# Performance work log

Measured on AMD Instinct MI355X. Metric: run time of the kernel, lower is better.

The kernel has to match this reference:

```python
import jax, jax.numpy as jnp
import numpy as np

T, C, H = 2048, 1024, 16
D = C // H  # head dim = 64


def setup_inputs() -> dict:
    key = jax.random.key(0)
    k1, k2, k3 = jax.random.split(key, 3)
    x = jax.random.normal(k1, (T, C), dtype=jnp.float32)
    W_qkv = jax.random.normal(k2, (C, 3 * C), dtype=jnp.float32) * (1.0 / np.sqrt(C))
    b_qkv = jnp.zeros((3 * C,), dtype=jnp.float32)
    W_proj = jax.random.normal(k3, (C, C), dtype=jnp.float32) * (1.0 / np.sqrt(C))
    b_proj = jnp.zeros((C,), dtype=jnp.float32)
    return {"x": x, "W_qkv": W_qkv, "b_qkv": b_qkv, "W_proj": W_proj, "b_proj": b_proj}


def reference(x, W_qkv, b_qkv, W_proj, b_proj):
    t, c = x.shape
    qkv = x @ W_qkv + b_qkv                      # [T, 3C] fused QKV projection
    q, k, v = jnp.split(qkv, 3, axis=-1)         # each [T, C]
    # split heads: [T, C] -> [H, T, D]
    q = q.reshape(t, H, D).transpose(1, 0, 2)
    k = k.reshape(t, H, D).transpose(1, 0, 2)
    v = v.reshape(t, H, D).transpose(1, 0, 2)
    # naive O(T^2) attention, full score matrix [H, T, T]
    att = jnp.einsum('htd,hsd->hts', q, k) / jnp.sqrt(jnp.float32(D))
    att = jax.nn.softmax(att, axis=-1)
    y = jnp.einsum('hts,hsd->htd', att, v)       # [H, T, D]
    y = y.transpose(1, 0, 2).reshape(t, c)       # merge heads -> [T, C]
    return y @ W_proj + b_proj
```

## Files before the change

### kernel.cpp

```cpp
#include <hip/hip_runtime.h>
#include <hip/hip_bf16.h>
#include <stdint.h>

#define T_DIM 2048
#define C_DIM 1024
#define H_DIM 16
#define D_HEAD 64
#define N_QKV 3072
#define CQ 0.18033688011112042f

typedef __bf16 bf16;
typedef __bf16 bf16x8 __attribute__((ext_vector_type(8)));
typedef __bf16 bf16x4 __attribute__((ext_vector_type(4)));
typedef __bf16 bf16x2 __attribute__((ext_vector_type(2)));
typedef float f32x4 __attribute__((ext_vector_type(4)));
typedef short s16x4 __attribute__((ext_vector_type(4)));

__device__ __forceinline__ void lds_load16(const void* g, void* l) {
    __builtin_amdgcn_global_load_lds(
        (const __attribute__((address_space(1))) void*)g,
        (__attribute__((address_space(3))) void*)l, 16, 0, 0);
}

__device__ __forceinline__ f32x4 mfma16(bf16x4 a, bf16x4 b, f32x4 c) {
#if __has_builtin(__builtin_amdgcn_mfma_f32_16x16x16_bf16)
    return __builtin_amdgcn_mfma_f32_16x16x16_bf16(a, b, c, 0, 0, 0);
#elif __has_builtin(__builtin_amdgcn_mfma_f32_16x16x16bf16_1k)
    union { bf16x4 v; s16x4 s; } ua, ub;
    ua.v = a; ub.v = b;
    return __builtin_amdgcn_mfma_f32_16x16x16bf16_1k(ua.s, ub.s, c, 0, 0, 0);
#else
    asm volatile("v_mfma_f32_16x16x16_bf16 %0, %1, %2, %0"
                 : "+v"(c) : "v"(a), "v"(b));
    return c;
#endif
}

__global__ void prep_kernel(const float* __restrict__ x, bf16* __restrict__ xb,
                            const float* __restrict__ Wq, bf16* __restrict__ WqT,
                            const float* __restrict__ Wp, bf16* __restrict__ WpT) {
    __shared__ float tile[32][33];
    int bid = blockIdx.x;
    int t = threadIdx.x;
    if (bid < 1024) {
        int i = (bid * 256 + t) * 8;
        float4 a = *(const float4*)(x + i);
        float4 b = *(const float4*)(x + i + 4);
        bf16x8 o;
        o[0] = (bf16)a.x; o[1] = (bf16)a.y; o[2] = (bf16)a.z; o[3] = (bf16)a.w;
        o[4] = (bf16)b.x; o[5] = (bf16)b.y; o[6] = (bf16)b.z; o[7] = (bf16)b.w;
        *(bf16x8*)(xb + i) = o;
        return;
    }
    bid -= 1024;
    const float* in; bf16* out; int N, nb, kb;
    if (bid < 3072) { in = Wq; out = WqT; N = N_QKV; nb = (bid % 96) * 32; kb = (bid / 96) * 32; }
    else { bid -= 3072; in = Wp; out = WpT; N = C_DIM; nb = (bid % 32) * 32; kb = (bid / 32) * 32; }
    int r = t >> 3, c4 = (t & 7) * 4;
    float4 v = *(const float4*)(in + (size_t)(kb + r) * N + nb + c4);
    tile[r][c4 + 0] = v.x; tile[r][c4 + 1] = v.y;
    tile[r][c4 + 2] = v.z; tile[r][c4 + 3] = v.w;
    __syncthreads();
    bf16x4 ov;
    ov[0] = (bf16)tile[c4 + 0][r]; ov[1] = (bf16)tile[c4 + 1][r];
    ov[2] = (bf16)tile[c4 + 2][r]; ov[3] = (bf16)tile[c4 + 3][r];
    *(bf16x4*)(out + (size_t)(nb + r) * C_DIM + kb + c4) = ov;
}

#define QKV_STAGE(BUF, K0) do {                                                      \
    lds_load16(ga + (K0),                            &As[BUF][0][(w * 16) * 32]);    \
    lds_load16(ga + (K0) + 32,                       &As[BUF][1][(w * 16) * 32]);    \
    lds_load16(ga + (size_t)64 * C_DIM + (K0),       &As[BUF][0][(64 + w * 16) * 32]); \
    lds_load16(ga + (size_t)64 * C_DIM + (K0) + 32,  &As[BUF][1][(64 + w * 16) * 32]); \
    lds_load16(gb + (K0),                            &Bs[BUF][0][(w * 16) * 32]);    \
    lds_load16(gb + (K0) + 32,                       &Bs[BUF][1][(w * 16) * 32]);    \
    lds_load16(gb + (size_t)64 * C_DIM + (K0),       &Bs[BUF][0][(64 + w * 16) * 32]); \
    lds_load16(gb + (size_t)64 * C_DIM + (K0) + 32,  &Bs[BUF][1][(64 + w * 16) * 32]); \
} while (0)

#define QKV_COMPUTE(BUF) do {                                                \
    _Pragma("unroll")                                                        \
    for (int p = 0; p < 2; ++p) {                                            \
        bf16x8 af[4], bfr[4];                                                \
        _Pragma("unroll")                                                    \
        for (int mi = 0; mi < 4; ++mi) af[mi]  = *(const bf16x8*)&As[BUF][p][(wm + mi * 16 + lo16) * 32 + quad * 8]; \
        _Pragma("unroll")                                                    \
        for (int ni = 0; ni < 4; ++ni) bfr[ni] = *(const bf16x8*)&Bs[BUF][p][(wn + ni * 16 + lo16) * 32 + quad * 8]; \
        _Pragma("unroll")                                                    \
        for (int mi = 0; mi < 4; ++mi)                                       \
            _Pragma("unroll")                                                \
            for (int ni = 0; ni < 4; ++ni)                                   \
                acc[mi][ni] = __builtin_amdgcn_mfma_f32_16x16x32_bf16(af[mi], bfr[ni], acc[mi][ni], 0, 0, 0); \
    }                                                                        \
} while (0)

#define WAIT_AND_BARRIER() do {                                              \
    asm volatile("s_waitcnt vmcnt(0)" ::: "memory");                         \
    __builtin_amdgcn_s_barrier();                                            \
} while (0)

__global__ __launch_bounds__(256, 2) void qkv_gemm_kernel(
    const bf16* __restrict__ A, const bf16* __restrict__ Bt,
    const float* __restrict__ bias, bf16* __restrict__ qkv)
{
    __shared__ __align__(16) bf16 As[2][2][128 * 32];
    __shared__ __align__(16) bf16 Bs[2][2][128 * 32];
    const int bid = blockIdx.x;
    const int xcd = bid & 7, slot = bid >> 3;
    const int rowBase = (slot / 3) * 128;
    const int colBase = (xcd * 3 + (slot % 3)) * 128;
    const int tid = threadIdx.x, lane = tid & 63, w = tid >> 6;
    const int lo16 = lane & 15, quad = lane >> 4;
    const int wm = (w & 1) * 64, wn = (w >> 1) * 64;

    const bf16* ga = A  + (size_t)(rowBase + w * 16 + (lane >> 2)) * C_DIM + (lane & 3) * 8;
    const bf16* gb = Bt + (size_t)(colBase + w * 16 + (lane >> 2)) * C_DIM + (lane & 3) * 8;

    f32x4 acc[4][4] = {};

    QKV_STAGE(0, 0);
    WAIT_AND_BARRIER();

    for (int k0 = 0; k0 < C_DIM; k0 += 128) {
        QKV_STAGE(1, k0 + 64);
        QKV_COMPUTE(0);
        WAIT_AND_BARRIER();
        if (k0 + 128 < C_DIM) QKV_STAGE(0, k0 + 128);
        QKV_COMPUTE(1);
        WAIT_AND_BARRIER();
    }

    const float scale = (colBase < C_DIM) ? CQ : 1.0f;
    #pragma unroll
    for (int ni = 0; ni < 4; ++ni) {
        int col = colBase + wn + ni * 16 + lo16;
        float bv = bias[col];
        #pragma unroll
        for (int mi = 0; mi < 4; ++mi) {
            int row0 = rowBase + wm + mi * 16 + quad * 4;
            #pragma unroll
            for (int r = 0; r < 4; ++r)
                qkv[(size_t)(row0 + r) * N_QKV + col] = (bf16)((acc[mi][ni][r] + bv) * scale);
        }
    }
}

#define NKT (T_DIM / 128)

#define FLASH_IT(KT, VC, VN)                                                          \
    {                                                                                 \
        bf16x8 nkf0 = kf0, nkf1 = kf1;                                                \
        if ((KT) + 1 < NKT) {                                                         \
            const bf16* kp = kfb + (size_t)((KT) + 1) * 128 * N_QKV;                  \
            nkf0 = *(const bf16x8*)(kp);                                              \
            nkf1 = *(const bf16x8*)(kp + 32);                                         \
            const bf16* vp = vfb + (size_t)((KT) + 1) * 128 * N_QKV;                  \
            _Pragma("unroll")                                                         \
            for (int mi = 0; mi < 4; ++mi)                                            \
                _Pragma("unroll")                                                     \
                for (int i = 0; i < 4; ++i)                                           \
                    VN[mi][i] = vp[(size_t)i * N_QKV + mi * 16];                      \
        }                                                                             \
        f32x4 st[4];                                                                  \
        __builtin_amdgcn_s_setprio(1);                                                \
        _Pragma("unroll")                                                             \
        for (int nq = 0; nq < 4; ++nq) {                                              \
            f32x4 z = {};                                                             \
            z = __builtin_amdgcn_mfma_f32_16x16x32_bf16(kf0, qf[nq][0], z, 0, 0, 0);  \
            st[nq] = __builtin_amdgcn_mfma_f32_16x16x32_bf16(kf1, qf[nq][1], z, 0, 0, 0); \
        }                                                                             \
        __builtin_amdgcn_s_setprio(0);                                                \
        bf16x4 pb[4];                                                                 \
        _Pragma("unroll")                                                             \
        for (int nq = 0; nq < 4; ++nq)                                                \
            _Pragma("unroll")                                                         \
            for (int r = 0; r < 4; ++r)                                               \
                pb[nq][r] = (bf16)__builtin_amdgcn_exp2f(st[nq][r]);                  \
        __builtin_amdgcn_s_setprio(1);                                                \
        _Pragma("unroll")                                                             \
        for (int nq = 0; nq < 4; ++nq)                                                \
            o_l[nq] = mfma16(pb[nq], ones1, o_l[nq]);                                 \
        _Pragma("unroll")                                                             \
        for (int nq = 0; nq < 4; ++nq)                                                \
            _Pragma("unroll")                                                         \
            for (int mi = 0; mi < 4; ++mi)                                            \
                o_t[nq][mi] = mfma16(pb[nq], VC[mi], o_t[nq][mi]);                    \
        __builtin_amdgcn_s_setprio(0);                                                \
        kf0 = nkf0; kf1 = nkf1;                                                       \
    }

__global__ __launch_bounds__(512, 2) void flash_kernel(
    const bf16* __restrict__ qkv,
    bf16* __restrict__ y)
{
    __shared__ float Ored[8][16][67];
    __shared__ float lred[8][64];

    const int bid = blockIdx.x;
    const int xcd = bid & 7, slot = bid >> 3;
    const int h = xcd * 2 + (slot & 1);
    const int qb = slot >> 1;
    const int tid  = threadIdx.x;
    const int lane = tid & 63, w = tid >> 6;
    const int lo16 = lane & 15, quad = lane >> 4;

    bf16x8 qf[4][2];
    #pragma unroll
    for (int nq = 0; nq < 4; ++nq)
        #pragma unroll
        for (int dk = 0; dk < 2; ++dk)
            qf[nq][dk] = *(const bf16x8*)(qkv + (size_t)(qb * 64 + nq * 16 + lo16) * N_QKV
                                          + h * D_HEAD + dk * 32 + quad * 8);

    f32x4 o_t[4][4] = {};
    f32x4 o_l[4] = {};
    bf16x4 ones1;
    ones1[0] = (bf16)1.0f; ones1[1] = (bf16)1.0f; ones1[2] = (bf16)1.0f; ones1[3] = (bf16)1.0f;

    const bf16* kfb = qkv + (size_t)(w * 16 + lo16) * N_QKV + C_DIM + h * D_HEAD + quad * 8;
    const bf16* vfb = qkv + (size_t)(w * 16 + quad * 4) * N_QKV + 2 * C_DIM + h * D_HEAD + lo16;

    bf16x8 kf0 = *(const bf16x8*)(kfb);
    bf16x8 kf1 = *(const bf16x8*)(kfb + 32);
    bf16x4 vA[4], vB[4];
    #pragma unroll
    for (int mi = 0; mi < 4; ++mi)
        #pragma unroll
        for (int i = 0; i < 4; ++i)
            vA[mi][i] = vfb[(size_t)i * N_QKV + mi * 16];

    for (int kt = 0; kt < NKT; kt += 2) {
        FLASH_IT(kt,     vA, vB);
        FLASH_IT(kt + 1, vB, vA);
    }

    if (lo16 == 0) {
        #pragma unroll
        for (int nq = 0; nq < 4; ++nq)
            #pragma unroll
            for (int i = 0; i < 4; ++i)
                lred[w][nq * 16 + quad * 4 + i] = o_l[nq][i];
    }

    const int qloc = tid >> 5;
    const int d0   = (tid & 31) * 2;
    for (int nq = 0; nq < 4; ++nq) {
        __syncthreads();
        #pragma unroll
        for (int mi = 0; mi < 4; ++mi)
            #pragma unroll
            for (int i = 0; i < 4; ++i)
                Ored[w][quad * 4 + i][mi * 16 + lo16] = o_t[nq][mi][i];
        __syncthreads();
        float ls = 0.f;
        #pragma unroll
        for (int j = 0; j < 8; ++j) ls += lred[j][nq * 16 + qloc];
        float linv = 1.0f / ls;
        float s0 = 0.f, s1 = 0.f;
        #pragma unroll
        for (int j = 0; j < 8; ++j) { s0 += Ored[j][qloc][d0]; s1 += Ored[j][qloc][d0 + 1]; }
        bf16x2 ov;
        ov[0] = (bf16)(s0 * linv); ov[1] = (bf16)(s1 * linv);
        *(bf16x2*)&y[(size_t)(qb * 64 + nq * 16 + qloc) * C_DIM + h * D_HEAD + d0] = ov;
    }
}

#define PROJ_STAGE(BUF, K0) do {                                             \
    lds_load16(ga + (K0),      &As[BUF][0][(w * 16) * 32]);                  \
    lds_load16(ga + (K0) + 32, &As[BUF][1][(w * 16) * 32]);                  \
    lds_load16(gb + (K0),      &Bs[BUF][0][(w * 16) * 32]);                  \
    lds_load16(gb + (K0) + 32, &Bs[BUF][1][(w * 16) * 32]);                  \
} while (0)

#define PROJ_COMPUTE(BUF) do {                                               \
    _Pragma("unroll")                                                        \
    for (int p = 0; p < 2; ++p) {                                            \
        bf16x8 af[2], bfr[2];                                                \
        _Pragma("unroll")                                                    \
        for (int mi = 0; mi < 2; ++mi) af[mi]  = *(const bf16x8*)&As[BUF][p][(wm + mi * 16 + lo16) * 32 + quad * 8]; \
        _Pragma("unroll")                                                    \
        for (int ni = 0; ni < 2; ++ni) bfr[ni] = *(const bf16x8*)&Bs[BUF][p][(wn + ni * 16 + lo16) * 32 + quad * 8]; \
        _Pragma("unroll")                                                    \
        for (int mi = 0; mi < 2; ++mi)                                       \
            _Pragma("unroll")                                                \
            for (int ni = 0; ni < 2; ++ni)                                   \
                acc[mi][ni] = __builtin_amdgcn_mfma_f32_16x16x32_bf16(af[mi], bfr[ni], acc[mi][ni], 0, 0, 0); \
    }                                                                        \
} while (0)

__global__ __launch_bounds__(256, 4) void proj_gemm_kernel(
    const bf16* __restrict__ A, const bf16* __restrict__ Bt,
    const float* __restrict__ bias, float* __restrict__ out)
{
    __shared__ __align__(16) bf16 As[2][2][64 * 32];
    __shared__ __align__(16) bf16 Bs[2][2][64 * 32];
    const int bid = blockIdx.x;
    const int xcd = bid & 7, slot = bid >> 3;
    const int colBase = (xcd * 2 + (slot & 1)) * 64;
    const int rowBase = (slot >> 1) * 64;
    const int tid = threadIdx.x, lane = tid & 63, w = tid >> 6;
    const int lo16 = lane & 15, quad = lane >> 4;
    const int wm = (w & 1) * 32, wn = (w >> 1) * 32;

    const bf16* ga = A  + (size_t)(rowBase + w * 16 + (lane >> 2)) * C_DIM + (lane & 3) * 8;
    const bf16* gb = Bt + (size_t)(colBase + w * 16 + (lane >> 2)) * C_DIM + (lane & 3) * 8;

    f32x4 acc[2][2] = {};

    PROJ_STAGE(0, 0);
    WAIT_AND_BARRIER();

    for (int k0 = 0; k0 < C_DIM; k0 += 128) {
        PROJ_STAGE(1, k0 + 64);
        PROJ_COMPUTE(0);
        WAIT_AND_BARRIER();
        if (k0 + 128 < C_DIM) PROJ_STAGE(0, k0 + 128);
        PROJ_COMPUTE(1);
        WAIT_AND_BARRIER();
    }

    #pragma unroll
    for (int ni = 0; ni < 2; ++ni) {
        int col = colBase + wn + ni * 16 + lo16;
        float bv = bias[col];
        #pragma unroll
        for (int mi = 0; mi < 2; ++mi) {
            int row0 = rowBase + wm + mi * 16 + quad * 4;
            #pragma unroll
            for (int r = 0; r < 4; ++r)
                out[(size_t)(row0 + r) * C_DIM + col] = acc[mi][ni][r] + bv;
        }
    }
}

extern "C" void kernel_launch(void* const* d_in, const int* in_sizes, int n_in,
                              void* d_out, int out_size, void* d_ws, size_t ws_size,
                              hipStream_t stream) {
    const float* x      = (const float*)d_in[0];
    const float* W_qkv  = (const float*)d_in[1];
    const float* b_qkv  = (const float*)d_in[2];
    const float* W_proj = (const float*)d_in[3];
    const float* b_proj = (const float*)d_in[4];
    float* out = (float*)d_out;

    char* ws = (char*)d_ws;
    bf16* xb      = (bf16*)(ws);
    bf16* Wqkv_t  = (bf16*)(ws + (4  << 20));
    bf16* Wproj_t = (bf16*)(ws + (10 << 20));
    bf16* qkv_bf  = (bf16*)(ws + (12 << 20));
    bf16* yb      = (bf16*)(ws + (24 << 20));

    prep_kernel<<<5120, 256, 0, stream>>>(x, xb, W_qkv, Wqkv_t, W_proj, Wproj_t);

    qkv_gemm_kernel<<<384, 256, 0, stream>>>(xb, Wqkv_t, b_qkv, qkv_bf);

    flash_kernel<<<512, 512, 0, stream>>>(qkv_bf, yb);

    proj_gemm_kernel<<<512, 256, 0, stream>>>(yb, Wproj_t, b_proj, out);
}
```

Measured before the change: 150.2 us.

## Write V transposed from QKV GEMM epilogue for vectorized flash V loads

```diff
diff --git a/kernel.cpp b/kernel.cpp
--- a/kernel.cpp
+++ b/kernel.cpp
@@ -101,7 +101,8 @@
 
 __global__ __launch_bounds__(256, 2) void qkv_gemm_kernel(
     const bf16* __restrict__ A, const bf16* __restrict__ Bt,
-    const float* __restrict__ bias, bf16* __restrict__ qkv)
+    const float* __restrict__ bias, bf16* __restrict__ qkv,
+    bf16* __restrict__ vT)
 {
     __shared__ __align__(16) bf16 As[2][2][128 * 32];
     __shared__ __align__(16) bf16 Bs[2][2][128 * 32];
@@ -130,17 +131,34 @@
         WAIT_AND_BARRIER();
     }
 
-    const float scale = (colBase < C_DIM) ? CQ : 1.0f;
-    #pragma unroll
-    for (int ni = 0; ni < 4; ++ni) {
-        int col = colBase + wn + ni * 16 + lo16;
-        float bv = bias[col];
-        #pragma unroll
-        for (int mi = 0; mi < 4; ++mi) {
-            int row0 = rowBase + wm + mi * 16 + quad * 4;
-            #pragma unroll
-            for (int r = 0; r < 4; ++r)
-                qkv[(size_t)(row0 + r) * N_QKV + col] = (bf16)((acc[mi][ni][r] + bv) * scale);
+    if (colBase < 2 * C_DIM) {
+        const float scale = (colBase < C_DIM) ? CQ : 1.0f;
+        #pragma unroll
+        for (int ni = 0; ni < 4; ++ni) {
+            int col = colBase + wn + ni * 16 + lo16;
+            float bv = bias[col];
+            #pragma unroll
+            for (int mi = 0; mi < 4; ++mi) {
+                int row0 = rowBase + wm + mi * 16 + quad * 4;
+                #pragma unroll
+                for (int r = 0; r < 4; ++r)
+                    qkv[(size_t)(row0 + r) * N_QKV + col] = (bf16)((acc[mi][ni][r] + bv) * scale);
+            }
+        }
+    } else {
+        #pragma unroll
+        for (int ni = 0; ni < 4; ++ni) {
+            int col = colBase + wn + ni * 16 + lo16;
+            int vc = col - 2 * C_DIM;
+            float bv = bias[col];
+            #pragma unroll
+            for (int mi = 0; mi < 4; ++mi) {
+                int row0 = rowBase + wm + mi * 16 + quad * 4;
+                bf16x4 ov;
+                #pragma unroll
+                for (int r = 0; r < 4; ++r) ov[r] = (bf16)(acc[mi][ni][r] + bv);
+                *(bf16x4*)&vT[(size_t)vc * T_DIM + row0] = ov;
+            }
         }
     }
 }
@@ -154,12 +172,10 @@
             const bf16* kp = kfb + (size_t)((KT) + 1) * 128 * N_QKV;                  \
             nkf0 = *(const bf16x8*)(kp);                                              \
             nkf1 = *(const bf16x8*)(kp + 32);                                         \
-            const bf16* vp = vfb + (size_t)((KT) + 1) * 128 * N_QKV;                  \
+            const bf16* vp = vfb + ((KT) + 1) * 128;                                  \
             _Pragma("unroll")                                                         \
             for (int mi = 0; mi < 4; ++mi)                                            \
-                _Pragma("unroll")                                                     \
-                for (int i = 0; i < 4; ++i)                                           \
-                    VN[mi][i] = vp[(size_t)i * N_QKV + mi * 16];                      \
+                VN[mi] = *(const bf16x4*)(vp + mi * 16 * T_DIM);                      \
         }                                                                             \
         f32x4 st[4];                                                                  \
         __builtin_amdgcn_s_setprio(1);                                                \
@@ -191,6 +207,7 @@
 
 __global__ __launch_bounds__(512, 2) void flash_kernel(
     const bf16* __restrict__ qkv,
+    const bf16* __restrict__ vT,
     bf16* __restrict__ y)
 {
     __shared__ float Ored[8][16][67];
@@ -218,16 +235,14 @@
     ones1[0] = (bf16)1.0f; ones1[1] = (bf16)1.0f; ones1[2] = (bf16)1.0f; ones1[3] = (bf16)1.0f;
 
     const bf16* kfb = qkv + (size_t)(w * 16 + lo16) * N_QKV + C_DIM + h * D_HEAD + quad * 8;
-    const bf16* vfb = qkv + (size_t)(w * 16 + quad * 4) * N_QKV + 2 * C_DIM + h * D_HEAD + lo16;
+    const bf16* vfb = vT + ((size_t)h * D_HEAD + lo16) * T_DIM + w * 16 + quad * 4;
 
     bf16x8 kf0 = *(const bf16x8*)(kfb);
     bf16x8 kf1 = *(const bf16x8*)(kfb + 32);
     bf16x4 vA[4], vB[4];
     #pragma unroll
     for (int mi = 0; mi < 4; ++mi)
-        #pragma unroll
-        for (int i = 0; i < 4; ++i)
-            vA[mi][i] = vfb[(size_t)i * N_QKV + mi * 16];
+        vA[mi] = *(const bf16x4*)(vfb + mi * 16 * T_DIM);
 
     for (int kt = 0; kt < NKT; kt += 2) {
         FLASH_IT(kt,     vA, vB);
@@ -349,12 +364,13 @@
     bf16* Wproj_t = (bf16*)(ws + (10 << 20));
     bf16* qkv_bf  = (bf16*)(ws + (12 << 20));
     bf16* yb      = (bf16*)(ws + (24 << 20));
+    bf16* vT      = (bf16*)(ws + (28 << 20));
 
     prep_kernel<<<5120, 256, 0, stream>>>(x, xb, W_qkv, Wqkv_t, W_proj, Wproj_t);
 
-    qkv_gemm_kernel<<<384, 256, 0, stream>>>(xb, Wqkv_t, b_qkv, qkv_bf);
-
-    flash_kernel<<<512, 512, 0, stream>>>(qkv_bf, yb);
+    qkv_gemm_kernel<<<384, 256, 0, stream>>>(xb, Wqkv_t, b_qkv, qkv_bf, vT);
+
+    flash_kernel<<<512, 512, 0, stream>>>(qkv_bf, vT, yb);
 
     proj_gemm_kernel<<<512, 256, 0, stream>>>(yb, Wproj_t, b_proj, out);
 }
```

Result: slower. 169.6 us (+12.9%).

## Rebalance QKV GEMM tiles, fold W_proj transpose into it, shrink flash blocks

Applied to the files above, without the earlier changes.

```diff
diff --git a/kernel.cpp b/kernel.cpp
--- a/kernel.cpp
+++ b/kernel.cpp
@@ -37,8 +37,7 @@
 }
 
 __global__ void prep_kernel(const float* __restrict__ x, bf16* __restrict__ xb,
-                            const float* __restrict__ Wq, bf16* __restrict__ WqT,
-                            const float* __restrict__ Wp, bf16* __restrict__ WpT) {
+                            const float* __restrict__ Wq, bf16* __restrict__ WqT) {
     __shared__ float tile[32][33];
     int bid = blockIdx.x;
     int t = threadIdx.x;
@@ -53,18 +52,16 @@
         return;
     }
     bid -= 1024;
-    const float* in; bf16* out; int N, nb, kb;
-    if (bid < 3072) { in = Wq; out = WqT; N = N_QKV; nb = (bid % 96) * 32; kb = (bid / 96) * 32; }
-    else { bid -= 3072; in = Wp; out = WpT; N = C_DIM; nb = (bid % 32) * 32; kb = (bid / 32) * 32; }
+    int nb = (bid % 96) * 32, kb = (bid / 96) * 32;
     int r = t >> 3, c4 = (t & 7) * 4;
-    float4 v = *(const float4*)(in + (size_t)(kb + r) * N + nb + c4);
+    float4 v = *(const float4*)(Wq + (size_t)(kb + r) * N_QKV + nb + c4);
     tile[r][c4 + 0] = v.x; tile[r][c4 + 1] = v.y;
     tile[r][c4 + 2] = v.z; tile[r][c4 + 3] = v.w;
     __syncthreads();
     bf16x4 ov;
     ov[0] = (bf16)tile[c4 + 0][r]; ov[1] = (bf16)tile[c4 + 1][r];
     ov[2] = (bf16)tile[c4 + 2][r]; ov[3] = (bf16)tile[c4 + 3][r];
-    *(bf16x4*)(out + (size_t)(nb + r) * C_DIM + kb + c4) = ov;
+    *(bf16x4*)(WqT + (size_t)(nb + r) * C_DIM + kb + c4) = ov;
 }
 
 #define QKV_STAGE(BUF, K0) do {                                                      \
@@ -74,22 +71,24 @@
     lds_load16(ga + (size_t)64 * C_DIM + (K0) + 32,  &As[BUF][1][(64 + w * 16) * 32]); \
     lds_load16(gb + (K0),                            &Bs[BUF][0][(w * 16) * 32]);    \
     lds_load16(gb + (K0) + 32,                       &Bs[BUF][1][(w * 16) * 32]);    \
-    lds_load16(gb + (size_t)64 * C_DIM + (K0),       &Bs[BUF][0][(64 + w * 16) * 32]); \
-    lds_load16(gb + (size_t)64 * C_DIM + (K0) + 32,  &Bs[BUF][1][(64 + w * 16) * 32]); \
+    if (w < 2) {                                                                     \
+        lds_load16(gb + (size_t)64 * C_DIM + (K0),      &Bs[BUF][0][(64 + w * 16) * 32]); \
+        lds_load16(gb + (size_t)64 * C_DIM + (K0) + 32, &Bs[BUF][1][(64 + w * 16) * 32]); \
+    }                                                                                \
 } while (0)
 
 #define QKV_COMPUTE(BUF) do {                                                \
     _Pragma("unroll")                                                        \
     for (int p = 0; p < 2; ++p) {                                            \
-        bf16x8 af[4], bfr[4];                                                \
+        bf16x8 af[4], bfr[3];                                                \
         _Pragma("unroll")                                                    \
         for (int mi = 0; mi < 4; ++mi) af[mi]  = *(const bf16x8*)&As[BUF][p][(wm + mi * 16 + lo16) * 32 + quad * 8]; \
         _Pragma("unroll")                                                    \
-        for (int ni = 0; ni < 4; ++ni) bfr[ni] = *(const bf16x8*)&Bs[BUF][p][(wn + ni * 16 + lo16) * 32 + quad * 8]; \
+        for (int ni = 0; ni < 3; ++ni) bfr[ni] = *(const bf16x8*)&Bs[BUF][p][(wn + ni * 16 + lo16) * 32 + quad * 8]; \
         _Pragma("unroll")                                                    \
         for (int mi = 0; mi < 4; ++mi)                                       \
             _Pragma("unroll")                                                \
-            for (int ni = 0; ni < 4; ++ni)                                   \
+            for (int ni = 0; ni < 3; ++ni)                                   \
                 acc[mi][ni] = __builtin_amdgcn_mfma_f32_16x16x32_bf16(af[mi], bfr[ni], acc[mi][ni], 0, 0, 0); \
     }                                                                        \
 } while (0)
@@ -101,22 +100,58 @@
 
 __global__ __launch_bounds__(256, 2) void qkv_gemm_kernel(
     const bf16* __restrict__ A, const bf16* __restrict__ Bt,
-    const float* __restrict__ bias, bf16* __restrict__ qkv)
+    const float* __restrict__ bias, bf16* __restrict__ qkv,
+    const float* __restrict__ Wp, bf16* __restrict__ WpT)
 {
-    __shared__ __align__(16) bf16 As[2][2][128 * 32];
-    __shared__ __align__(16) bf16 Bs[2][2][128 * 32];
+    __shared__ union {
+        struct {
+            __align__(16) bf16 As[2][2][128 * 32];
+            __align__(16) bf16 Bs[2][2][96 * 32];
+        } g;
+        float tile[64][65];
+    } u;
     const int bid = blockIdx.x;
+    const int tid = threadIdx.x;
+
+    if (bid >= 512) {
+        int b2 = bid - 512;
+        int nb = (b2 & 15) * 64, kb = (b2 >> 4) * 64;
+        {
+            int r = tid >> 2, c16 = (tid & 3) * 16;
+            const float* src = Wp + (size_t)(kb + r) * C_DIM + nb + c16;
+            #pragma unroll
+            for (int j = 0; j < 4; ++j) {
+                float4 v = *(const float4*)(src + j * 4);
+                u.tile[r][c16 + j * 4 + 0] = v.x; u.tile[r][c16 + j * 4 + 1] = v.y;
+                u.tile[r][c16 + j * 4 + 2] = v.z; u.tile[r][c16 + j * 4 + 3] = v.w;
+            }
+        }
+        __syncthreads();
+        {
+            int n = tid >> 2, s = (tid & 3) * 16;
+            bf16x8 o0, o1;
+            #pragma unroll
+            for (int j = 0; j < 8; ++j) { o0[j] = (bf16)u.tile[s + j][n]; o1[j] = (bf16)u.tile[s + 8 + j][n]; }
+            bf16* dst = WpT + (size_t)(nb + n) * C_DIM + kb + s;
+            *(bf16x8*)(dst)     = o0;
+            *(bf16x8*)(dst + 8) = o1;
+        }
+        return;
+    }
+
+    auto& As = u.g.As;
+    auto& Bs = u.g.Bs;
     const int xcd = bid & 7, slot = bid >> 3;
-    const int rowBase = (slot / 3) * 128;
-    const int colBase = (xcd * 3 + (slot % 3)) * 128;
-    const int tid = threadIdx.x, lane = tid & 63, w = tid >> 6;
+    const int rowBase = (slot >> 2) * 128;
+    const int colBase = (xcd * 4 + (slot & 3)) * 96;
+    const int lane = tid & 63, w = tid >> 6;
     const int lo16 = lane & 15, quad = lane >> 4;
-    const int wm = (w & 1) * 64, wn = (w >> 1) * 64;
+    const int wm = (w & 1) * 64, wn = (w >> 1) * 48;
 
     const bf16* ga = A  + (size_t)(rowBase + w * 16 + (lane >> 2)) * C_DIM + (lane & 3) * 8;
     const bf16* gb = Bt + (size_t)(colBase + w * 16 + (lane >> 2)) * C_DIM + (lane & 3) * 8;
 
-    f32x4 acc[4][4] = {};
+    f32x4 acc[4][3] = {};
 
     QKV_STAGE(0, 0);
     WAIT_AND_BARRIER();
@@ -130,10 +165,10 @@
         WAIT_AND_BARRIER();
     }
 
-    const float scale = (colBase < C_DIM) ? CQ : 1.0f;
-    #pragma unroll
-    for (int ni = 0; ni < 4; ++ni) {
+    #pragma unroll
+    for (int ni = 0; ni < 3; ++ni) {
         int col = colBase + wn + ni * 16 + lo16;
+        const float scale = (col < C_DIM) ? CQ : 1.0f;
         float bv = bias[col];
         #pragma unroll
         for (int mi = 0; mi < 4; ++mi) {
@@ -145,43 +180,43 @@
     }
 }
 
-#define NKT (T_DIM / 128)
+#define NKT (T_DIM / 64)
 
 #define FLASH_IT(KT, VC, VN)                                                          \
     {                                                                                 \
         bf16x8 nkf0 = kf0, nkf1 = kf1;                                                \
         if ((KT) + 1 < NKT) {                                                         \
-            const bf16* kp = kfb + (size_t)((KT) + 1) * 128 * N_QKV;                  \
+            const bf16* kp = kfb + (size_t)((KT) + 1) * 64 * N_QKV;                   \
             nkf0 = *(const bf16x8*)(kp);                                              \
             nkf1 = *(const bf16x8*)(kp + 32);                                         \
-            const bf16* vp = vfb + (size_t)((KT) + 1) * 128 * N_QKV;                  \
+            const bf16* vp = vfb + (size_t)((KT) + 1) * 64 * N_QKV;                   \
             _Pragma("unroll")                                                         \
             for (int mi = 0; mi < 4; ++mi)                                            \
                 _Pragma("unroll")                                                     \
                 for (int i = 0; i < 4; ++i)                                           \
                     VN[mi][i] = vp[(size_t)i * N_QKV + mi * 16];                      \
         }                                                                             \
-        f32x4 st[4];                                                                  \
+        f32x4 st[2];                                                                  \
         __builtin_amdgcn_s_setprio(1);                                                \
         _Pragma("unroll")                                                             \
-        for (int nq = 0; nq < 4; ++nq) {                                              \
+        for (int nq = 0; nq < 2; ++nq) {                                              \
             f32x4 z = {};                                                             \
             z = __builtin_amdgcn_mfma_f32_16x16x32_bf16(kf0, qf[nq][0], z, 0, 0, 0);  \
             st[nq] = __builtin_amdgcn_mfma_f32_16x16x32_bf16(kf1, qf[nq][1], z, 0, 0, 0); \
         }                                                                             \
         __builtin_amdgcn_s_setprio(0);                                                \
-        bf16x4 pb[4];                                                                 \
+        bf16x4 pb[2];                                                                 \
         _Pragma("unroll")                                                             \
-        for (int nq = 0; nq < 4; ++nq)                                                \
+        for (int nq = 0; nq < 2; ++nq)                                                \
             _Pragma("unroll")                                                         \
             for (int r = 0; r < 4; ++r)                                               \
                 pb[nq][r] = (bf16)__builtin_amdgcn_exp2f(st[nq][r]);                  \
         __builtin_amdgcn_s_setprio(1);                                                \
         _Pragma("unroll")                                                             \
-        for (int nq = 0; nq < 4; ++nq)                                                \
+        for (int nq = 0; nq < 2; ++nq)                                                \
             o_l[nq] = mfma16(pb[nq], ones1, o_l[nq]);                                 \
         _Pragma("unroll")                                                             \
-        for (int nq = 0; nq < 4; ++nq)                                                \
+        for (int nq = 0; nq < 2; ++nq)                                                \
             _Pragma("unroll")                                                         \
             for (int mi = 0; mi < 4; ++mi)                                            \
                 o_t[nq][mi] = mfma16(pb[nq], VC[mi], o_t[nq][mi]);                    \
@@ -189,12 +224,12 @@
         kf0 = nkf0; kf1 = nkf1;                                                       \
     }
 
-__global__ __launch_bounds__(512, 2) void flash_kernel(
+__global__ __launch_bounds__(256, 4) void flash_kernel(
     const bf16* __restrict__ qkv,
     bf16* __restrict__ y)
 {
-    __shared__ float Ored[8][16][67];
-    __shared__ float lred[8][64];
+    __shared__ float Ored[4][16][67];
+    __shared__ float lred[4][32];
 
     const int bid = blockIdx.x;
     const int xcd = bid & 7, slot = bid >> 3;
@@ -204,16 +239,16 @@
     const int lane = tid & 63, w = tid >> 6;
     const int lo16 = lane & 15, quad = lane >> 4;
 
-    bf16x8 qf[4][2];
-    #pragma unroll
-    for (int nq = 0; nq < 4; ++nq)
+    bf16x8 qf[2][2];
+    #pragma unroll
+    for (int nq = 0; nq < 2; ++nq)
         #pragma unroll
         for (int dk = 0; dk < 2; ++dk)
-            qf[nq][dk] = *(const bf16x8*)(qkv + (size_t)(qb * 64 + nq * 16 + lo16) * N_QKV
+            qf[nq][dk] = *(const bf16x8*)(qkv + (size_t)(qb * 32 + nq * 16 + lo16) * N_QKV
                                           + h * D_HEAD + dk * 32 + quad * 8);
 
-    f32x4 o_t[4][4] = {};
-    f32x4 o_l[4] = {};
+    f32x4 o_t[2][4] = {};
+    f32x4 o_l[2] = {};
     bf16x4 ones1;
     ones1[0] = (bf16)1.0f; ones1[1] = (bf16)1.0f; ones1[2] = (bf16)1.0f; ones1[3] = (bf16)1.0f;
 
@@ -236,15 +271,16 @@
 
     if (lo16 == 0) {
         #pragma unroll
-        for (int nq = 0; nq < 4; ++nq)
+        for (int nq = 0; nq < 2; ++nq)
             #pragma unroll
             for (int i = 0; i < 4; ++i)
                 lred[w][nq * 16 + quad * 4 + i] = o_l[nq][i];
     }
 
-    const int qloc = tid >> 5;
-    const int d0   = (tid & 31) * 2;
-    for (int nq = 0; nq < 4; ++nq) {
+    const int qloc = tid >> 4;
+    const int d0   = (tid & 15) * 4;
+    #pragma unroll
+    for (int nq = 0; nq < 2; ++nq) {
         __syncthreads();
         #pragma unroll
         for (int mi = 0; mi < 4; ++mi)
@@ -254,14 +290,17 @@
         __syncthreads();
         float ls = 0.f;
         #pragma unroll
-        for (int j = 0; j < 8; ++j) ls += lred[j][nq * 16 + qloc];
+        for (int j = 0; j < 4; ++j) ls += lred[j][nq * 16 + qloc];
         float linv = 1.0f / ls;
-        float s0 = 0.f, s1 = 0.f;
-        #pragma unroll
-        for (int j = 0; j < 8; ++j) { s0 += Ored[j][qloc][d0]; s1 += Ored[j][qloc][d0 + 1]; }
-        bf16x2 ov;
-        ov[0] = (bf16)(s0 * linv); ov[1] = (bf16)(s1 * linv);
-        *(bf16x2*)&y[(size_t)(qb * 64 + nq * 16 + qloc) * C_DIM + h * D_HEAD + d0] = ov;
+        bf16x4 ov;
+        #pragma unroll
+        for (int di = 0; di < 4; ++di) {
+            float s = 0.f;
+            #pragma unroll
+            for (int j = 0; j < 4; ++j) s += Ored[j][qloc][d0 + di];
+            ov[di] = (bf16)(s * linv);
+        }
+        *(bf16x4*)&y[(size_t)(qb * 32 + nq * 16 + qloc) * C_DIM + h * D_HEAD + d0] = ov;
     }
 }
 
@@ -350,11 +389,11 @@
     bf16* qkv_bf  = (bf16*)(ws + (12 << 20));
     bf16* yb      = (bf16*)(ws + (24 << 20));
 
-    prep_kernel<<<5120, 256, 0, stream>>>(x, xb, W_qkv, Wqkv_t, W_proj, Wproj_t);
-
-    qkv_gemm_kernel<<<384, 256, 0, stream>>>(xb, Wqkv_t, b_qkv, qkv_bf);
-
-    flash_kernel<<<512, 512, 0, stream>>>(qkv_bf, yb);
+    prep_kernel<<<4096, 256, 0, stream>>>(x, xb, W_qkv, Wqkv_t);
+
+    qkv_gemm_kernel<<<768, 256, 0, stream>>>(xb, Wqkv_t, b_qkv, qkv_bf, W_proj, Wproj_t);
+
+    flash_kernel<<<1024, 256, 0, stream>>>(qkv_bf, yb);
 
     proj_gemm_kernel<<<512, 256, 0, stream>>>(yb, Wproj_t, b_proj, out);
 }
```

New measurement: 156.5 us. 1.04x slower.
